# Kernel tuning notes

Hardware: AMD Instinct MI355X
Metric: run time of the kernel (lower is better)

Reference implementation:

```python
import jax, jax.numpy as jnp
import numpy as np

B, T, D_MODEL, HEADS = 2, 2048, 1024, 16
D_HEAD = D_MODEL // HEADS


def setup_inputs() -> dict:
    key = jax.random.key(0)
    ks = jax.random.split(key, 9)
    s = 1.0 / np.sqrt(D_HEAD)
    return {
        "x": jax.random.normal(ks[0], (B, T, D_MODEL), dtype=jnp.float32),
        "Wq": jax.random.normal(ks[1], (D_HEAD, D_HEAD), dtype=jnp.float32) * s,
        "bq": jax.random.normal(ks[2], (D_HEAD,), dtype=jnp.float32) * 0.01,
        "Wk": jax.random.normal(ks[3], (D_HEAD, D_HEAD), dtype=jnp.float32) * s,
        "bk": jax.random.normal(ks[4], (D_HEAD,), dtype=jnp.float32) * 0.01,
        "Wv": jax.random.normal(ks[5], (D_HEAD, D_HEAD), dtype=jnp.float32) * s,
        "bv": jax.random.normal(ks[6], (D_HEAD,), dtype=jnp.float32) * 0.01,
        "Wp": jax.random.normal(ks[7], (D_MODEL, D_MODEL), dtype=jnp.float32) * (1.0 / np.sqrt(D_MODEL)),
        "bp": jax.random.normal(ks[8], (D_MODEL,), dtype=jnp.float32) * 0.01,
    }


def reference(x, Wq, bq, Wk, bk, Wv, bv, Wp, bp):
    b, t, c = x.shape
    xh = x.reshape(b, t, HEADS, D_HEAD)  # [B,T,H,dh]
    # per-head linear projections (weights shared across heads), nn.Linear: y = x @ W.T + b
    q = jnp.einsum('bthd,ed->bhte', xh, Wq) + bq  # [B,H,T,dh]
    k = jnp.einsum('bthd,ed->bhte', xh, Wk) + bk
    v = jnp.einsum('bthd,ed->bhte', xh, Wv) + bv
    # NOTE: original scales by sqrt(C) = sqrt(d_model), not sqrt(d_head)
    scale = 1.0 / jnp.sqrt(jnp.float32(c))
    att = jnp.einsum('bhqd,bhkd->bhqk', q, k) * scale  # [B,H,T,T]
    att = jax.nn.softmax(att, axis=-1)
    out = jnp.einsum('bhqk,bhkd->bhqd', att, v)  # [B,H,T,dh]
    out = out.transpose(0, 2, 1, 3).reshape(b, t, c)  # [B,T,C]
    out = out @ Wp.T + bp
    return out
```

## Files before the change

kernel.cpp:

```cpp
#include <hip/hip_runtime.h>
#include <hip/hip_bf16.h>

#define B_ 2
#define T_ 2048
#define DM_ 1024
#define H_ 16
#define DH_ 64
#define QSCALE 0.045084220027780106f

typedef unsigned short u16;
typedef unsigned int u32;
typedef __attribute__((ext_vector_type(2))) unsigned int u32x2;
typedef __attribute__((ext_vector_type(4))) unsigned int u32x4;
typedef __attribute__((ext_vector_type(4))) float f32x4v;
typedef __attribute__((ext_vector_type(8))) short bf16x8;
typedef __attribute__((ext_vector_type(4))) float f32x4;
typedef __attribute__((ext_vector_type(16))) float f32x16;

__device__ __forceinline__ u16 f2bf(float f) {
    u32 u = __float_as_uint(f);
    return (u16)((u + 0x7FFF + ((u >> 16) & 1)) >> 16);
}
__device__ __forceinline__ float bf2f(u16 h) {
    return __uint_as_float(((u32)h) << 16);
}
__device__ __forceinline__ float exp2_fast(float x) {
    float r;
    asm("v_exp_f32 %0, %1" : "=v"(r) : "v"(x));
    return r;
}
__device__ __forceinline__ u32 cvtpk_bf16(float lo, float hi) {
    u32 r;
    asm("v_cvt_pk_bf16_f32 %0, %1, %2" : "=v"(r) : "v"(lo), "v"(hi));
    return r;
}

__device__ __forceinline__ const bf16x8* frag_at(const u16* base, int row, int c16) {
    return (const bf16x8*)((const char*)base + row * 128 + ((c16 ^ (row & 7)) << 4));
}

__global__ __launch_bounds__(256) void wsplit_all(
    const float* __restrict__ Wq, const float* __restrict__ Wk,
    const float* __restrict__ Wv, const float* __restrict__ Wp,
    u16* __restrict__ W6, u16* __restrict__ Wh, u16* __restrict__ Wl)
{
    const int i = blockIdx.x * 256 + threadIdx.x;
    if (i < DM_ * DM_) {
        const float w = Wp[i];
        const u16 hi = f2bf(w);
        Wh[i] = hi;
        Wl[i] = f2bf(w - bf2f(hi));
    } else {
        const int j = i - DM_ * DM_;
        const int mat = j >> 12, idx = j & 4095;
        const float w = (mat == 0) ? Wq[idx] : (mat == 1) ? Wk[idx] : Wv[idx];
        const u16 hi = f2bf(w);
        W6[(mat * 2) * 4096 + idx] = hi;
        W6[(mat * 2 + 1) * 4096 + idx] = f2bf(w - bf2f(hi));
    }
}

__global__ __launch_bounds__(256) void qkv_mfma(
    const float* __restrict__ x,
    const float* __restrict__ bq, const float* __restrict__ bk,
    const float* __restrict__ bv, const u16* __restrict__ W6,
    u16* __restrict__ Q, u16* __restrict__ K, u16* __restrict__ VT)
{
    __shared__ u16 Ws[6 * 4096];

    const int tid = threadIdx.x;
    const int wid = tid >> 6;
    const int lane = tid & 63;
    const int li = lane & 15, g = lane >> 4;

    const int bh = blockIdx.x >> 4;
    const int t0 = (blockIdx.x & 15) * 128;
    const int b = bh >> 4, h = bh & 15;
    const int tw0 = t0 + wid * 32;

    #pragma unroll
    for (int j = 0; j < 12; ++j) {
        const int gi = j * 256 + tid;
        const int tile = gi >> 9;
        const int t16 = gi & 511;
        const int r = t16 >> 3, c16 = t16 & 7;
        const int c16s = c16 ^ (r & 7);
        __builtin_amdgcn_global_load_lds(
            (const __attribute__((address_space(1))) u32*)((const char*)W6 + tile * 8192 + r * 128 + (c16s << 4)),
            (__attribute__((address_space(3))) u32*)((char*)Ws + gi * 16),
            16, 0, 0);
    }

    const float* xb = x + ((size_t)b * T_) * DM_ + h * 64;
    f32x4v xr[2][2][2];
    #pragma unroll
    for (int mt = 0; mt < 2; ++mt)
        #pragma unroll
        for (int kt = 0; kt < 2; ++kt) {
            const float* p = xb + (size_t)(tw0 + 16 * mt + li) * DM_ + kt * 32 + g * 8;
            xr[mt][kt][0] = *(const f32x4v*)p;
            xr[mt][kt][1] = *(const f32x4v*)(p + 4);
        }

    float bq_r[4], bk_r[4], bv_r[4][4];
    #pragma unroll
    for (int nt = 0; nt < 4; ++nt) { bq_r[nt] = bq[16 * nt + li]; bk_r[nt] = bk[16 * nt + li]; }
    #pragma unroll
    for (int vd = 0; vd < 4; ++vd)
        #pragma unroll
        for (int rg = 0; rg < 4; ++rg) bv_r[vd][rg] = bv[16 * vd + 4 * g + rg];

    __syncthreads();

    bf16x8 xhf[2][2], xlf[2][2];
    #pragma unroll
    for (int mt = 0; mt < 2; ++mt)
        #pragma unroll
        for (int kt = 0; kt < 2; ++kt) {
            u32 hw[4], lw[4];
            #pragma unroll
            for (int q2 = 0; q2 < 2; ++q2) {
                const f32x4v v = xr[mt][kt][q2];
                const u32 p0 = cvtpk_bf16(v[0], v[1]);
                const u32 p1 = cvtpk_bf16(v[2], v[3]);
                const float l0 = v[0] - __uint_as_float(p0 << 16);
                const float l1 = v[1] - __uint_as_float(p0 & 0xFFFF0000u);
                const float l2 = v[2] - __uint_as_float(p1 << 16);
                const float l3 = v[3] - __uint_as_float(p1 & 0xFFFF0000u);
                hw[q2 * 2] = p0; hw[q2 * 2 + 1] = p1;
                lw[q2 * 2] = cvtpk_bf16(l0, l1);
                lw[q2 * 2 + 1] = cvtpk_bf16(l2, l3);
            }
            xhf[mt][kt] = *(const bf16x8*)hw;
            xlf[mt][kt] = *(const bf16x8*)lw;
        }

    const u16* Wqh = Ws;
    const u16* Wql = Ws + 4096;
    const u16* Wkh = Ws + 8192;
    const u16* Wkl = Ws + 12288;
    const u16* Wvh = Ws + 16384;
    const u16* Wvl = Ws + 20480;

    const size_t qk_base = ((size_t)bh * T_) * DH_;

    {
        f32x4 acc[2][4];
        #pragma unroll
        for (int mt = 0; mt < 2; ++mt)
            #pragma unroll
            for (int nt = 0; nt < 4; ++nt) acc[mt][nt] = (f32x4){0.f, 0.f, 0.f, 0.f};
        #pragma unroll
        for (int nt = 0; nt < 4; ++nt)
            #pragma unroll
            for (int kt = 0; kt < 2; ++kt) {
                const bf16x8 wh = *frag_at(Wqh, 16 * nt + li, 4 * kt + g);
                const bf16x8 wl = *frag_at(Wql, 16 * nt + li, 4 * kt + g);
                #pragma unroll
                for (int mt = 0; mt < 2; ++mt) {
                    acc[mt][nt] = __builtin_amdgcn_mfma_f32_16x16x32_bf16(xhf[mt][kt], wh, acc[mt][nt], 0, 0, 0);
                    acc[mt][nt] = __builtin_amdgcn_mfma_f32_16x16x32_bf16(xlf[mt][kt], wh, acc[mt][nt], 0, 0, 0);
                    acc[mt][nt] = __builtin_amdgcn_mfma_f32_16x16x32_bf16(xhf[mt][kt], wl, acc[mt][nt], 0, 0, 0);
                }
            }
        #pragma unroll
        for (int mt = 0; mt < 2; ++mt)
            #pragma unroll
            for (int rg = 0; rg < 4; ++rg) {
                const int t = tw0 + 16 * mt + 4 * g + rg;
                #pragma unroll
                for (int nt = 0; nt < 4; ++nt)
                    Q[qk_base + (size_t)t * DH_ + 16 * nt + li] =
                        f2bf((acc[mt][nt][rg] + bq_r[nt]) * QSCALE);
            }
    }

    {
        f32x4 acc[2][4];
        #pragma unroll
        for (int mt = 0; mt < 2; ++mt)
            #pragma unroll
            for (int nt = 0; nt < 4; ++nt) acc[mt][nt] = (f32x4){0.f, 0.f, 0.f, 0.f};
        #pragma unroll
        for (int nt = 0; nt < 4; ++nt)
            #pragma unroll
            for (int kt = 0; kt < 2; ++kt) {
                const bf16x8 wh = *frag_at(Wkh, 16 * nt + li, 4 * kt + g);
                const bf16x8 wl = *frag_at(Wkl, 16 * nt + li, 4 * kt + g);
                #pragma unroll
                for (int mt = 0; mt < 2; ++mt) {
                    acc[mt][nt] = __builtin_amdgcn_mfma_f32_16x16x32_bf16(xhf[mt][kt], wh, acc[mt][nt], 0, 0, 0);
                    acc[mt][nt] = __builtin_amdgcn_mfma_f32_16x16x32_bf16(xlf[mt][kt], wh, acc[mt][nt], 0, 0, 0);
                    acc[mt][nt] = __builtin_amdgcn_mfma_f32_16x16x32_bf16(xhf[mt][kt], wl, acc[mt][nt], 0, 0, 0);
                }
            }
        #pragma unroll
        for (int mt = 0; mt < 2; ++mt)
            #pragma unroll
            for (int rg = 0; rg < 4; ++rg) {
                const int t = tw0 + 16 * mt + 4 * g + rg;
                #pragma unroll
                for (int nt = 0; nt < 4; ++nt)
                    K[qk_base + (size_t)t * DH_ + 16 * nt + li] =
                        f2bf(acc[mt][nt][rg] + bk_r[nt]);
            }
    }

    {
        f32x4 acc[4][2];
        #pragma unroll
        for (int vd = 0; vd < 4; ++vd)
            #pragma unroll
            for (int tc = 0; tc < 2; ++tc) acc[vd][tc] = (f32x4){0.f, 0.f, 0.f, 0.f};
        #pragma unroll
        for (int vd = 0; vd < 4; ++vd)
            #pragma unroll
            for (int kt = 0; kt < 2; ++kt) {
                const bf16x8 ah = *frag_at(Wvh, 16 * vd + li, 4 * kt + g);
                const bf16x8 al = *frag_at(Wvl, 16 * vd + li, 4 * kt + g);
                #pragma unroll
                for (int tc = 0; tc < 2; ++tc) {
                    acc[vd][tc] = __builtin_amdgcn_mfma_f32_16x16x32_bf16(ah, xhf[tc][kt], acc[vd][tc], 0, 0, 0);
                    acc[vd][tc] = __builtin_amdgcn_mfma_f32_16x16x32_bf16(al, xhf[tc][kt], acc[vd][tc], 0, 0, 0);
                    acc[vd][tc] = __builtin_amdgcn_mfma_f32_16x16x32_bf16(ah, xlf[tc][kt], acc[vd][tc], 0, 0, 0);
                }
            }
        u16* VTb = VT + (size_t)bh * DH_ * T_;
        #pragma unroll
        for (int vd = 0; vd < 4; ++vd)
            #pragma unroll
            for (int rg = 0; rg < 4; ++rg) {
                const int d = 16 * vd + 4 * g + rg;
                #pragma unroll
                for (int tc = 0; tc < 2; ++tc)
                    VTb[(size_t)d * T_ + tw0 + 16 * tc + li] =
                        f2bf(acc[vd][tc][rg] + bv_r[vd][rg]);
            }
    }
}

__global__ __launch_bounds__(256) void attn_mfma(
    const u16* __restrict__ Q, const u16* __restrict__ K,
    const u16* __restrict__ VT, u16* __restrict__ Ah, u16* __restrict__ Al)
{
    __shared__ char smem[32768];

    const int tid = threadIdx.x;
    const int wid = tid >> 6;
    const int lane = tid & 63;
    const int l = lane & 31, h = lane >> 5;
    const int flat = blockIdx.x;
    const int bh = (flat & 7) + ((flat >> 7) << 3);
    const int qx = (flat >> 3) & 15;
    const int q0 = qx * 128 + wid * 32;

    const size_t bhoff = (size_t)bh * T_ * DH_;

    bf16x8 qf[4];
    {
        const u16* Qp = Q + bhoff + (size_t)(q0 + l) * DH_ + 8 * h;
        #pragma unroll
        for (int kt = 0; kt < 4; ++kt)
            qf[kt] = *(const bf16x8*)(Qp + 16 * kt);
    }

    f32x16 o0 = {}, o1 = {};
    float l_part = 0.f;

    const char* ldsR[4];
    #pragma unroll
    for (int kt = 0; kt < 4; ++kt)
        ldsR[kt] = smem + l * 128 + ((((2 * kt + h) ^ (l & 7))) << 4);

    const int sl_r = lane >> 3;
    const int sl_c = (lane & 7) ^ sl_r;
    const char* kgp0 = (const char*)(K + bhoff) + (16 * wid + sl_r) * 128 + (sl_c << 4);
    const char* kgp1 = kgp0 + 8 * 128;
    const char* vgp0 = (const char*)(VT + (size_t)bh * DH_ * T_) + (size_t)(16 * wid + sl_r) * (T_ * 2) + (sl_c << 4);
    const char* vgp1 = vgp0 + (size_t)8 * (T_ * 2);
    const int kdst = 16 * wid * 128 + lane * 16;

#define STAGE(BUF)                                                                       \
    {                                                                                    \
        __builtin_amdgcn_global_load_lds(                                                \
            (const __attribute__((address_space(1))) u32*)kgp0,                          \
            (__attribute__((address_space(3))) u32*)(smem + (BUF) + kdst), 16, 0, 0);    \
        __builtin_amdgcn_global_load_lds(                                                \
            (const __attribute__((address_space(1))) u32*)kgp1,                          \
            (__attribute__((address_space(3))) u32*)(smem + (BUF) + kdst + 1024), 16, 0, 0); \
        __builtin_amdgcn_global_load_lds(                                                \
            (const __attribute__((address_space(1))) u32*)vgp0,                          \
            (__attribute__((address_space(3))) u32*)(smem + 16384 + (BUF) + kdst), 16, 0, 0); \
        __builtin_amdgcn_global_load_lds(                                                \
            (const __attribute__((address_space(1))) u32*)vgp1,                          \
            (__attribute__((address_space(3))) u32*)(smem + 16384 + (BUF) + kdst + 1024), 16, 0, 0); \
        kgp0 += 8192; kgp1 += 8192; vgp0 += 128; vgp1 += 128;                            \
    }

#define ATTN_ITER(BUF, DO_PREF)                                                          \
    {                                                                                    \
        __syncthreads();                                                                 \
        if (DO_PREF) STAGE((BUF) ^ 8192);                                                \
        f32x16 s0 = {}, s1 = {};                                                         \
        __builtin_amdgcn_s_setprio(1);                                                   \
        _Pragma("unroll")                                                                \
        for (int kt = 0; kt < 4; ++kt) {                                                 \
            const bf16x8 kf0 = *(const bf16x8*)(ldsR[kt] + (BUF));                       \
            const bf16x8 kf1 = *(const bf16x8*)(ldsR[kt] + (BUF) + 4096);                \
            s0 = __builtin_amdgcn_mfma_f32_32x32x16_bf16(kf0, qf[kt], s0, 0, 0, 0);      \
            s1 = __builtin_amdgcn_mfma_f32_32x32x16_bf16(kf1, qf[kt], s1, 0, 0, 0);      \
        }                                                                                \
        __builtin_amdgcn_s_setprio(0);                                                   \
        float lacc = 0.f;                                                                \
        _Pragma("unroll")                                                                \
        for (int r = 0; r < 16; ++r) { s0[r] = exp2_fast(s0[r]); lacc += s0[r]; }        \
        _Pragma("unroll")                                                                \
        for (int r = 0; r < 16; ++r) { s1[r] = exp2_fast(s1[r]); lacc += s1[r]; }        \
        l_part += lacc;                                                                  \
        __builtin_amdgcn_s_setprio(1);                                                   \
        _Pragma("unroll")                                                                \
        for (int kt = 0; kt < 4; ++kt) {                                                 \
            const int rb = (kt & 1) * 8;                                                 \
            u32 w0, w1, w2, w3;                                                          \
            if (kt < 2) {                                                                \
                w0 = cvtpk_bf16(s0[rb + 0], s0[rb + 1]);                                 \
                w1 = cvtpk_bf16(s0[rb + 2], s0[rb + 3]);                                 \
                w2 = cvtpk_bf16(s0[rb + 4], s0[rb + 5]);                                 \
                w3 = cvtpk_bf16(s0[rb + 6], s0[rb + 7]);                                 \
            } else {                                                                     \
                w0 = cvtpk_bf16(s1[rb + 0], s1[rb + 1]);                                 \
                w1 = cvtpk_bf16(s1[rb + 2], s1[rb + 3]);                                 \
                w2 = cvtpk_bf16(s1[rb + 4], s1[rb + 5]);                                 \
                w3 = cvtpk_bf16(s1[rb + 6], s1[rb + 7]);                                 \
            }                                                                            \
            asm("v_permlane32_swap_b32 %0, %1" : "+v"(w0), "+v"(w2));                    \
            asm("v_permlane32_swap_b32 %0, %1" : "+v"(w1), "+v"(w3));                    \
            u32x4 pw; pw[0] = w0; pw[1] = w1; pw[2] = w2; pw[3] = w3;                    \
            const bf16x8 pf = __builtin_bit_cast(bf16x8, pw);                            \
            const bf16x8 vf0 = *(const bf16x8*)(ldsR[kt] + 16384 + (BUF));               \
            const bf16x8 vf1 = *(const bf16x8*)(ldsR[kt] + 16384 + (BUF) + 4096);        \
            o0 = __builtin_amdgcn_mfma_f32_32x32x16_bf16(vf0, pf, o0, 0, 0, 0);          \
            o1 = __builtin_amdgcn_mfma_f32_32x32x16_bf16(vf1, pf, o1, 0, 0, 0);          \
        }                                                                                \
        __builtin_amdgcn_s_setprio(0);                                                   \
    }

    STAGE(0);
    for (int it = 0; it < 32; it += 2) {
        ATTN_ITER(0, true);
        ATTN_ITER(8192, (it + 2 < 32));
    }
#undef ATTN_ITER
#undef STAGE

    const float lt = l_part + __shfl_xor(l_part, 32);
    const float inv = 1.0f / lt;

    __syncthreads();

    char* ehi = smem + wid * 8192;
    char* elo = ehi + 4096;
    #pragma unroll
    for (int db = 0; db < 2; ++db) {
        #pragma unroll
        for (int rr = 0; rr < 4; ++rr) {
            float v0, v1, v2, v3;
            if (db == 0) {
                v0 = o0[4 * rr + 0] * inv; v1 = o0[4 * rr + 1] * inv;
                v2 = o0[4 * rr + 2] * inv; v3 = o0[4 * rr + 3] * inv;
            } else {
                v0 = o1[4 * rr + 0] * inv; v1 = o1[4 * rr + 1] * inv;
                v2 = o1[4 * rr + 2] * inv; v3 = o1[4 * rr + 3] * inv;
            }
            u32x2 wh, wl;
            wh.x = cvtpk_bf16(v0, v1);
            wh.y = cvtpk_bf16(v2, v3);
            const float r0 = v0 - __uint_as_float(wh.x << 16);
            const float r1 = v1 - __uint_as_float(wh.x & 0xFFFF0000u);
            const float r2 = v2 - __uint_as_float(wh.y << 16);
            const float r3 = v3 - __uint_as_float(wh.y & 0xFFFF0000u);
            wl.x = cvtpk_bf16(r0, r1);
            wl.y = cvtpk_bf16(r2, r3);
            const int byteoff = l * 128 + (((4 * db + rr) ^ (l & 7)) << 4) + 8 * h;
            *(u32x2*)(ehi + byteoff) = wh;
            *(u32x2*)(elo + byteoff) = wl;
        }
    }

    const int b = bh >> 4, head = bh & 15;
    const int sub = lane & 7;
    const int row8 = lane >> 3;
    #pragma unroll
    for (int rr = 0; rr < 4; ++rr) {
        const int row = 8 * rr + row8;
        const int byteoff = row * 128 + ((sub ^ row8) << 4);
        const size_t gidx = ((size_t)b * T_ + q0 + row) * DM_ + head * 64 + sub * 8;
        *(u32x4*)(Ah + gidx) = *(const u32x4*)(ehi + byteoff);
        *(u32x4*)(Al + gidx) = *(const u32x4*)(elo + byteoff);
    }
}

__global__ __launch_bounds__(512) void proj_mfma(
    const u16* __restrict__ Ah, const u16* __restrict__ Al,
    const u16* __restrict__ Wh, const u16* __restrict__ Wl,
    const float* __restrict__ bp, float* __restrict__ out)
{
    __shared__ char smem[131072];

    const int tid = threadIdx.x;
    const int wid = tid >> 6;
    const int lane = tid & 63;
    const int li = lane & 15, g = lane >> 4;
    const int row0 = blockIdx.y * 128, col0 = blockIdx.x * 128;

    const int mat = wid >> 1, half = wid & 1;
    const char* gsrc;
    if (mat == 0)      gsrc = (const char*)(Ah + (size_t)row0 * DM_);
    else if (mat == 1) gsrc = (const char*)(Al + (size_t)row0 * DM_);
    else if (mat == 2) gsrc = (const char*)(Wh + (size_t)col0 * DM_);
    else               gsrc = (const char*)(Wl + (size_t)col0 * DM_);
    const int r_local = half * 64 + (lane >> 3);
    const int c16s = (lane & 7) ^ (lane >> 3);
    const char* gp0 = gsrc + (size_t)r_local * (DM_ * 2) + (c16s << 4);
    const int ldst0 = mat * 16384 + half * 8192;

#define PSTAGE(BUF, STEP)                                                                \
    {                                                                                    \
        _Pragma("unroll")                                                                \
        for (int j = 0; j < 8; ++j) {                                                    \
            __builtin_amdgcn_global_load_lds(                                            \
                (const __attribute__((address_space(1))) u32*)(gp0 + (size_t)(STEP) * 128 + (size_t)j * (8 * DM_ * 2)), \
                (__attribute__((address_space(3))) u32*)(smem + (BUF) + ldst0 + j * 1024),\
                16, 0, 0);                                                               \
        }                                                                                \
    }

    const int wr = wid >> 1, wc = wid & 1;

    f32x4 acc[2][4];
    #pragma unroll
    for (int m = 0; m < 2; ++m)
        #pragma unroll
        for (int n = 0; n < 4; ++n) acc[m][n] = (f32x4){0.f, 0.f, 0.f, 0.f};

    PSTAGE(0, 0);
    for (int step = 0; step < 16; ++step) {
        const int buf = (step & 1) * 65536;
        __syncthreads();
        if (step < 15) PSTAGE(buf ^ 65536, step + 1);

        const u16* pAh = (const u16*)(smem + buf);
        const u16* pAl = (const u16*)(smem + buf + 16384);
        const u16* pWh = (const u16*)(smem + buf + 32768);
        const u16* pWl = (const u16*)(smem + buf + 49152);

        __builtin_amdgcn_s_setprio(1);
        #pragma unroll
        for (int kt = 0; kt < 2; ++kt) {
            bf16x8 ah[2], al[2], wh[4], wl[4];
            #pragma unroll
            for (int m = 0; m < 2; ++m) {
                ah[m] = *frag_at(pAh, wr * 32 + m * 16 + li, kt * 4 + g);
                al[m] = *frag_at(pAl, wr * 32 + m * 16 + li, kt * 4 + g);
            }
            #pragma unroll
            for (int n = 0; n < 4; ++n) {
                wh[n] = *frag_at(pWh, wc * 64 + n * 16 + li, kt * 4 + g);
                wl[n] = *frag_at(pWl, wc * 64 + n * 16 + li, kt * 4 + g);
            }
            #pragma unroll
            for (int m = 0; m < 2; ++m)
                #pragma unroll
                for (int n = 0; n < 4; ++n) {
                    acc[m][n] = __builtin_amdgcn_mfma_f32_16x16x32_bf16(ah[m], wh[n], acc[m][n], 0, 0, 0);
                    acc[m][n] = __builtin_amdgcn_mfma_f32_16x16x32_bf16(al[m], wh[n], acc[m][n], 0, 0, 0);
                    acc[m][n] = __builtin_amdgcn_mfma_f32_16x16x32_bf16(ah[m], wl[n], acc[m][n], 0, 0, 0);
                }
        }
        __builtin_amdgcn_s_setprio(0);
    }
#undef PSTAGE

    const int orow = row0 + wr * 32;
    const int ocol = col0 + wc * 64;
    float bias[4];
    #pragma unroll
    for (int n = 0; n < 4; ++n) bias[n] = bp[ocol + n * 16 + li];
    #pragma unroll
    for (int m = 0; m < 2; ++m)
        #pragma unroll
        for (int n = 0; n < 4; ++n)
            #pragma unroll
            for (int q = 0; q < 4; ++q)
                out[(size_t)(orow + m * 16 + g * 4 + q) * DM_ + ocol + n * 16 + li] =
                    acc[m][n][q] + bias[n];
}

extern "C" void kernel_launch(void* const* d_in, const int* in_sizes, int n_in,
                              void* d_out, int out_size, void* d_ws, size_t ws_size,
                              hipStream_t stream) {
    const float* x  = (const float*)d_in[0];
    const float* Wq = (const float*)d_in[1];
    const float* bq = (const float*)d_in[2];
    const float* Wk = (const float*)d_in[3];
    const float* bk = (const float*)d_in[4];
    const float* Wv = (const float*)d_in[5];
    const float* bv = (const float*)d_in[6];
    const float* Wp = (const float*)d_in[7];
    const float* bp = (const float*)d_in[8];
    float* out = (float*)d_out;

    const size_t n_qkv = (size_t)B_ * H_ * T_ * DH_;
    const size_t n_w   = (size_t)DM_ * DM_;
    u16* Qb  = (u16*)d_ws;
    u16* Kb  = Qb + n_qkv;
    u16* VTb = Kb + n_qkv;
    u16* Ahb = VTb + n_qkv;
    u16* Alb = Ahb + n_qkv;
    u16* Whb = Alb + n_qkv;
    u16* Wlb = Whb + n_w;
    u16* W6b = Wlb + n_w;

    wsplit_all<<<(n_w + 12288) / 256, 256, 0, stream>>>(Wq, Wk, Wv, Wp, W6b, Whb, Wlb);
    qkv_mfma<<<32 * 16, 256, 0, stream>>>(x, bq, bk, bv, W6b, Qb, Kb, VTb);
    attn_mfma<<<512, 256, 0, stream>>>(Qb, Kb, VTb, Ahb, Alb);
    proj_mfma<<<dim3(DM_ / 128, (B_ * T_) / 128), 512, 0, stream>>>(Ahb, Alb, Whb, Wlb, bp, out);
}
```

Baseline: 91.27 us.

## Split attention KV range across two blocks and add a combine kernel

Each attention block now covers half of the key/value sequence, so the grid doubles to 1024 blocks. Partial unnormalized outputs and row sums go to fp32 workspace, and a new combine kernel sums the halves, normalizes, and writes the hi/lo bf16 split, reusing the Q/K buffers as outputs. The main loop is also restructured to software-pipeline QK for the next tile with softmax/PV of the current one, using separate K and V staging. This raises occupancy and overlap at the cost of extra global traffic for the fp32 partials and one more kernel launch.

```diff
diff --git a/kernel.cpp b/kernel.cpp
--- a/kernel.cpp
+++ b/kernel.cpp
@@ -241,7 +241,7 @@
 
 __global__ __launch_bounds__(256) void attn_mfma(
     const u16* __restrict__ Q, const u16* __restrict__ K,
-    const u16* __restrict__ VT, u16* __restrict__ Ah, u16* __restrict__ Al)
+    const u16* __restrict__ VT, float* __restrict__ OP, float* __restrict__ LP)
 {
     __shared__ char smem[32768];
 
@@ -250,8 +250,9 @@
     const int lane = tid & 63;
     const int l = lane & 31, h = lane >> 5;
     const int flat = blockIdx.x;
-    const int bh = (flat & 7) + ((flat >> 7) << 3);
-    const int qx = (flat >> 3) & 15;
+    const int gid = flat & 63;
+    const int bh = gid >> 1, kvh = gid & 1;
+    const int qx = flat >> 6;
     const int q0 = qx * 128 + wid * 32;
 
     const size_t bhoff = (size_t)bh * T_ * DH_;
@@ -265,6 +266,7 @@
     }
 
     f32x16 o0 = {}, o1 = {};
+    f32x16 s0A = {}, s1A = {}, s0B = {}, s1B = {};
     float l_part = 0.f;
 
     const char* ldsR[4];
@@ -274,48 +276,55 @@
 
     const int sl_r = lane >> 3;
     const int sl_c = (lane & 7) ^ sl_r;
-    const char* kgp0 = (const char*)(K + bhoff) + (16 * wid + sl_r) * 128 + (sl_c << 4);
+    const char* kgp0 = (const char*)(K + bhoff) + kvh * 131072 + (16 * wid + sl_r) * 128 + (sl_c << 4);
     const char* kgp1 = kgp0 + 8 * 128;
-    const char* vgp0 = (const char*)(VT + (size_t)bh * DH_ * T_) + (size_t)(16 * wid + sl_r) * (T_ * 2) + (sl_c << 4);
+    const char* vgp0 = (const char*)(VT + (size_t)bh * DH_ * T_) + kvh * 2048 + (size_t)(16 * wid + sl_r) * (T_ * 2) + (sl_c << 4);
     const char* vgp1 = vgp0 + (size_t)8 * (T_ * 2);
     const int kdst = 16 * wid * 128 + lane * 16;
 
-#define STAGE(BUF)                                                                       \
+#define STAGE_K(DST)                                                                     \
     {                                                                                    \
         __builtin_amdgcn_global_load_lds(                                                \
             (const __attribute__((address_space(1))) u32*)kgp0,                          \
-            (__attribute__((address_space(3))) u32*)(smem + (BUF) + kdst), 16, 0, 0);    \
+            (__attribute__((address_space(3))) u32*)(smem + (DST) + kdst), 16, 0, 0);    \
         __builtin_amdgcn_global_load_lds(                                                \
             (const __attribute__((address_space(1))) u32*)kgp1,                          \
-            (__attribute__((address_space(3))) u32*)(smem + (BUF) + kdst + 1024), 16, 0, 0); \
+            (__attribute__((address_space(3))) u32*)(smem + (DST) + kdst + 1024), 16, 0, 0); \
+        kgp0 += 8192; kgp1 += 8192;                                                      \
+    }
+#define STAGE_V(DST)                                                                     \
+    {                                                                                    \
         __builtin_amdgcn_global_load_lds(                                                \
             (const __attribute__((address_space(1))) u32*)vgp0,                          \
-            (__attribute__((address_space(3))) u32*)(smem + 16384 + (BUF) + kdst), 16, 0, 0); \
+            (__attribute__((address_space(3))) u32*)(smem + (DST) + kdst), 16, 0, 0);    \
         __builtin_amdgcn_global_load_lds(                                                \
             (const __attribute__((address_space(1))) u32*)vgp1,                          \
-            (__attribute__((address_space(3))) u32*)(smem + 16384 + (BUF) + kdst + 1024), 16, 0, 0); \
-        kgp0 += 8192; kgp1 += 8192; vgp0 += 128; vgp1 += 128;                            \
-    }
-
-#define ATTN_ITER(BUF, DO_PREF)                                                          \
+            (__attribute__((address_space(3))) u32*)(smem + (DST) + kdst + 1024), 16, 0, 0); \
+        vgp0 += 128; vgp1 += 128;                                                        \
+    }
+
+#define QK_BLOCK(KB, S0, S1)                                                             \
     {                                                                                    \
-        __syncthreads();                                                                 \
-        if (DO_PREF) STAGE((BUF) ^ 8192);                                                \
-        f32x16 s0 = {}, s1 = {};                                                         \
+        S0 = (f32x16){}; S1 = (f32x16){};                                                \
         __builtin_amdgcn_s_setprio(1);                                                   \
         _Pragma("unroll")                                                                \
         for (int kt = 0; kt < 4; ++kt) {                                                 \
-            const bf16x8 kf0 = *(const bf16x8*)(ldsR[kt] + (BUF));                       \
-            const bf16x8 kf1 = *(const bf16x8*)(ldsR[kt] + (BUF) + 4096);                \
-            s0 = __builtin_amdgcn_mfma_f32_32x32x16_bf16(kf0, qf[kt], s0, 0, 0, 0);      \
-            s1 = __builtin_amdgcn_mfma_f32_32x32x16_bf16(kf1, qf[kt], s1, 0, 0, 0);      \
+            const bf16x8 kf0 = *(const bf16x8*)(ldsR[kt] + (KB));                        \
+            const bf16x8 kf1 = *(const bf16x8*)(ldsR[kt] + (KB) + 4096);                 \
+            S0 = __builtin_amdgcn_mfma_f32_32x32x16_bf16(kf0, qf[kt], S0, 0, 0, 0);      \
+            S1 = __builtin_amdgcn_mfma_f32_32x32x16_bf16(kf1, qf[kt], S1, 0, 0, 0);      \
         }                                                                                \
         __builtin_amdgcn_s_setprio(0);                                                   \
+        __builtin_amdgcn_sched_barrier(0);                                               \
+    }
+
+#define SOFTMAX_PV(S0, S1, VB)                                                           \
+    {                                                                                    \
         float lacc = 0.f;                                                                \
         _Pragma("unroll")                                                                \
-        for (int r = 0; r < 16; ++r) { s0[r] = exp2_fast(s0[r]); lacc += s0[r]; }        \
+        for (int r = 0; r < 16; ++r) { S0[r] = exp2_fast(S0[r]); lacc += S0[r]; }        \
         _Pragma("unroll")                                                                \
-        for (int r = 0; r < 16; ++r) { s1[r] = exp2_fast(s1[r]); lacc += s1[r]; }        \
+        for (int r = 0; r < 16; ++r) { S1[r] = exp2_fast(S1[r]); lacc += S1[r]; }        \
         l_part += lacc;                                                                  \
         __builtin_amdgcn_s_setprio(1);                                                   \
         _Pragma("unroll")                                                                \
@@ -323,81 +332,131 @@
             const int rb = (kt & 1) * 8;                                                 \
             u32 w0, w1, w2, w3;                                                          \
             if (kt < 2) {                                                                \
-                w0 = cvtpk_bf16(s0[rb + 0], s0[rb + 1]);                                 \
-                w1 = cvtpk_bf16(s0[rb + 2], s0[rb + 3]);                                 \
-                w2 = cvtpk_bf16(s0[rb + 4], s0[rb + 5]);                                 \
-                w3 = cvtpk_bf16(s0[rb + 6], s0[rb + 7]);                                 \
+                w0 = cvtpk_bf16(S0[rb + 0], S0[rb + 1]);                                 \
+                w1 = cvtpk_bf16(S0[rb + 2], S0[rb + 3]);                                 \
+                w2 = cvtpk_bf16(S0[rb + 4], S0[rb + 5]);                                 \
+                w3 = cvtpk_bf16(S0[rb + 6], S0[rb + 7]);                                 \
             } else {                                                                     \
-                w0 = cvtpk_bf16(s1[rb + 0], s1[rb + 1]);                                 \
-                w1 = cvtpk_bf16(s1[rb + 2], s1[rb + 3]);                                 \
-                w2 = cvtpk_bf16(s1[rb + 4], s1[rb + 5]);                                 \
-                w3 = cvtpk_bf16(s1[rb + 6], s1[rb + 7]);                                 \
+                w0 = cvtpk_bf16(S1[rb + 0], S1[rb + 1]);                                 \
+                w1 = cvtpk_bf16(S1[rb + 2], S1[rb + 3]);                                 \
+                w2 = cvtpk_bf16(S1[rb + 4], S1[rb + 5]);                                 \
+                w3 = cvtpk_bf16(S1[rb + 6], S1[rb + 7]);                                 \
             }                                                                            \
             asm("v_permlane32_swap_b32 %0, %1" : "+v"(w0), "+v"(w2));                    \
             asm("v_permlane32_swap_b32 %0, %1" : "+v"(w1), "+v"(w3));                    \
             u32x4 pw; pw[0] = w0; pw[1] = w1; pw[2] = w2; pw[3] = w3;                    \
             const bf16x8 pf = __builtin_bit_cast(bf16x8, pw);                            \
-            const bf16x8 vf0 = *(const bf16x8*)(ldsR[kt] + 16384 + (BUF));               \
-            const bf16x8 vf1 = *(const bf16x8*)(ldsR[kt] + 16384 + (BUF) + 4096);        \
+            const bf16x8 vf0 = *(const bf16x8*)(ldsR[kt] + (VB));                        \
+            const bf16x8 vf1 = *(const bf16x8*)(ldsR[kt] + (VB) + 4096);                 \
             o0 = __builtin_amdgcn_mfma_f32_32x32x16_bf16(vf0, pf, o0, 0, 0, 0);          \
             o1 = __builtin_amdgcn_mfma_f32_32x32x16_bf16(vf1, pf, o1, 0, 0, 0);          \
         }                                                                                \
         __builtin_amdgcn_s_setprio(0);                                                   \
     }
 
-    STAGE(0);
-    for (int it = 0; it < 32; it += 2) {
-        ATTN_ITER(0, true);
-        ATTN_ITER(8192, (it + 2 < 32));
-    }
-#undef ATTN_ITER
-#undef STAGE
+    STAGE_K(0);
+    STAGE_V(16384);
+    __syncthreads();
+    QK_BLOCK(0, s0A, s1A);
+    STAGE_K(8192);
+
+    for (int it = 0; it < 16; it += 2) {
+        __syncthreads();
+        if (it + 2 < 16) STAGE_K(0);
+        STAGE_V(24576);
+        QK_BLOCK(8192, s0B, s1B);
+        SOFTMAX_PV(s0A, s1A, 16384);
+
+        __syncthreads();
+        if (it + 3 < 16) STAGE_K(8192);
+        if (it + 2 < 16) {
+            STAGE_V(16384);
+            QK_BLOCK(0, s0A, s1A);
+        }
+        SOFTMAX_PV(s0B, s1B, 24576);
+    }
+#undef STAGE_K
+#undef STAGE_V
+#undef QK_BLOCK
+#undef SOFTMAX_PV
 
     const float lt = l_part + __shfl_xor(l_part, 32);
-    const float inv = 1.0f / lt;
 
     __syncthreads();
 
-    char* ehi = smem + wid * 8192;
-    char* elo = ehi + 4096;
+    float* ew = (float*)(smem + wid * 8192);
     #pragma unroll
     for (int db = 0; db < 2; ++db) {
         #pragma unroll
         for (int rr = 0; rr < 4; ++rr) {
-            float v0, v1, v2, v3;
+            f32x4v v;
             if (db == 0) {
-                v0 = o0[4 * rr + 0] * inv; v1 = o0[4 * rr + 1] * inv;
-                v2 = o0[4 * rr + 2] * inv; v3 = o0[4 * rr + 3] * inv;
+                v[0] = o0[4 * rr + 0]; v[1] = o0[4 * rr + 1];
+                v[2] = o0[4 * rr + 2]; v[3] = o0[4 * rr + 3];
             } else {
-                v0 = o1[4 * rr + 0] * inv; v1 = o1[4 * rr + 1] * inv;
-                v2 = o1[4 * rr + 2] * inv; v3 = o1[4 * rr + 3] * inv;
-            }
-            u32x2 wh, wl;
-            wh.x = cvtpk_bf16(v0, v1);
-            wh.y = cvtpk_bf16(v2, v3);
-            const float r0 = v0 - __uint_as_float(wh.x << 16);
-            const float r1 = v1 - __uint_as_float(wh.x & 0xFFFF0000u);
-            const float r2 = v2 - __uint_as_float(wh.y << 16);
-            const float r3 = v3 - __uint_as_float(wh.y & 0xFFFF0000u);
-            wl.x = cvtpk_bf16(r0, r1);
-            wl.y = cvtpk_bf16(r2, r3);
-            const int byteoff = l * 128 + (((4 * db + rr) ^ (l & 7)) << 4) + 8 * h;
-            *(u32x2*)(ehi + byteoff) = wh;
-            *(u32x2*)(elo + byteoff) = wl;
+                v[0] = o1[4 * rr + 0]; v[1] = o1[4 * rr + 1];
+                v[2] = o1[4 * rr + 2]; v[3] = o1[4 * rr + 3];
+            }
+            const int gr = (2 * rr + h + 8 * db) ^ (l & 15);
+            *(f32x4v*)((char*)ew + l * 256 + (gr << 4)) = v;
         }
     }
 
-    const int b = bh >> 4, head = bh & 15;
-    const int sub = lane & 7;
-    const int row8 = lane >> 3;
-    #pragma unroll
-    for (int rr = 0; rr < 4; ++rr) {
-        const int row = 8 * rr + row8;
-        const int byteoff = row * 128 + ((sub ^ row8) << 4);
-        const size_t gidx = ((size_t)b * T_ + q0 + row) * DM_ + head * 64 + sub * 8;
-        *(u32x4*)(Ah + gidx) = *(const u32x4*)(ehi + byteoff);
-        *(u32x4*)(Al + gidx) = *(const u32x4*)(elo + byteoff);
-    }
+    const size_t rowbase = (size_t)bh * T_ + q0;
+    float* opb = OP + (size_t)kvh * (65536ull * 64);
+    const int ql = lane >> 1, hf = lane & 1;
+    float* oprow = opb + (rowbase + ql) * 64 + hf * 32;
+    #pragma unroll
+    for (int j = 0; j < 8; ++j) {
+        const int gr = (hf * 8 + j) ^ (ql & 15);
+        const f32x4v v = *(const f32x4v*)((char*)ew + ql * 256 + (gr << 4));
+        *(f32x4v*)(oprow + 4 * j) = v;
+    }
+    if (h == 0) LP[kvh * 65536 + rowbase + l] = lt;
+}
+
+__global__ __launch_bounds__(256) void combine_kernel(
+    const float* __restrict__ OP, const float* __restrict__ LP,
+    u16* __restrict__ Ah, u16* __restrict__ Al)
+{
+    const int tid = threadIdx.x;
+    const int row = blockIdx.x * 64 + (tid >> 2);
+    const int dq = (tid & 3) * 16;
+    const float inv = 1.0f / (LP[row] + LP[65536 + row]);
+    const float* p0 = OP + (size_t)row * 64 + dq;
+    const float* p1 = p0 + 65536ull * 64;
+    const int bh = row >> 11, q = row & 2047;
+    const int b = bh >> 4, hh = bh & 15;
+    const size_t gidx = ((size_t)(b * T_ + q)) * DM_ + hh * 64 + dq;
+
+    u32 hw[8], lw[8];
+    #pragma unroll
+    for (int j = 0; j < 4; ++j) {
+        const f32x4v a = *(const f32x4v*)(p0 + 4 * j);
+        const f32x4v c = *(const f32x4v*)(p1 + 4 * j);
+        const float v0 = (a[0] + c[0]) * inv;
+        const float v1 = (a[1] + c[1]) * inv;
+        const float v2 = (a[2] + c[2]) * inv;
+        const float v3 = (a[3] + c[3]) * inv;
+        const u32 h0 = cvtpk_bf16(v0, v1);
+        const u32 h1 = cvtpk_bf16(v2, v3);
+        const float r0 = v0 - __uint_as_float(h0 << 16);
+        const float r1 = v1 - __uint_as_float(h0 & 0xFFFF0000u);
+        const float r2 = v2 - __uint_as_float(h1 << 16);
+        const float r3 = v3 - __uint_as_float(h1 & 0xFFFF0000u);
+        hw[2 * j] = h0; hw[2 * j + 1] = h1;
+        lw[2 * j] = cvtpk_bf16(r0, r1);
+        lw[2 * j + 1] = cvtpk_bf16(r2, r3);
+    }
+    u32x4 hv0, hv1, lv0, lv1;
+    hv0[0] = hw[0]; hv0[1] = hw[1]; hv0[2] = hw[2]; hv0[3] = hw[3];
+    hv1[0] = hw[4]; hv1[1] = hw[5]; hv1[2] = hw[6]; hv1[3] = hw[7];
+    lv0[0] = lw[0]; lv0[1] = lw[1]; lv0[2] = lw[2]; lv0[3] = lw[3];
+    lv1[0] = lw[4]; lv1[1] = lw[5]; lv1[2] = lw[6]; lv1[3] = lw[7];
+    *(u32x4*)(Ah + gidx) = hv0;
+    *(u32x4*)(Ah + gidx + 8) = hv1;
+    *(u32x4*)(Al + gidx) = lv0;
+    *(u32x4*)(Al + gidx + 8) = lv1;
 }
 
 __global__ __launch_bounds__(512) void proj_mfma(
@@ -515,14 +574,15 @@
     u16* Qb  = (u16*)d_ws;
     u16* Kb  = Qb + n_qkv;
     u16* VTb = Kb + n_qkv;
-    u16* Ahb = VTb + n_qkv;
-    u16* Alb = Ahb + n_qkv;
-    u16* Whb = Alb + n_qkv;
+    u16* Whb = VTb + n_qkv;
     u16* Wlb = Whb + n_w;
     u16* W6b = Wlb + n_w;
+    float* OPb = (float*)(W6b + 24576);
+    float* LPb = OPb + 2 * n_qkv;
 
     wsplit_all<<<(n_w + 12288) / 256, 256, 0, stream>>>(Wq, Wk, Wv, Wp, W6b, Whb, Wlb);
     qkv_mfma<<<32 * 16, 256, 0, stream>>>(x, bq, bk, bv, W6b, Qb, Kb, VTb);
-    attn_mfma<<<512, 256, 0, stream>>>(Qb, Kb, VTb, Ahb, Alb);
-    proj_mfma<<<dim3(DM_ / 128, (B_ * T_) / 128), 512, 0, stream>>>(Ahb, Alb, Whb, Wlb, bp, out);
-}
+    attn_mfma<<<1024, 256, 0, stream>>>(Qb, Kb, VTb, OPb, LPb);
+    combine_kernel<<<1024, 256, 0, stream>>>(OPb, LPb, Qb, Kb);
+    proj_mfma<<<dim3(DM_ / 128, (B_ * T_) / 128), 512, 0, stream>>>(Qb, Kb, Whb, Wlb, bp, out);
+}
```

New measurement: 106.5 us. 16.7% more time.

## Double the attention KV tile to 128 keys per iteration

Applied to the files above, without the earlier changes.

The attention main loop now processes 128 keys per iteration instead of 64. LDS doubles to 64KB to hold double-buffered K and V tiles, and the iteration count halves. This halves the number of block barriers and prefetch stages per key and exposes four independent QK MFMA chains before the softmax/PV phase. In exchange it adds register pressure from four live score accumulators, and the larger LDS footprint may cut the number of resident blocks per CU.

```diff
diff --git a/kernel.cpp b/kernel.cpp
--- a/kernel.cpp
+++ b/kernel.cpp
@@ -243,7 +243,7 @@
     const u16* __restrict__ Q, const u16* __restrict__ K,
     const u16* __restrict__ VT, u16* __restrict__ Ah, u16* __restrict__ Al)
 {
-    __shared__ char smem[32768];
+    __shared__ char smem[65536];
 
     const int tid = threadIdx.x;
     const int wid = tid >> 6;
@@ -265,92 +265,99 @@
     }
 
     f32x16 o0 = {}, o1 = {};
+    f32x16 sA, sB, sC, sD;
     float l_part = 0.f;
 
     const char* ldsR[4];
     #pragma unroll
-    for (int kt = 0; kt < 4; ++kt)
-        ldsR[kt] = smem + l * 128 + ((((2 * kt + h) ^ (l & 7))) << 4);
+    for (int j = 0; j < 4; ++j)
+        ldsR[j] = smem + l * 128 + ((((2 * j + h) ^ (l & 7))) << 4);
 
     const int sl_r = lane >> 3;
     const int sl_c = (lane & 7) ^ sl_r;
-    const char* kgp0 = (const char*)(K + bhoff) + (16 * wid + sl_r) * 128 + (sl_c << 4);
-    const char* kgp1 = kgp0 + 8 * 128;
-    const char* vgp0 = (const char*)(VT + (size_t)bh * DH_ * T_) + (size_t)(16 * wid + sl_r) * (T_ * 2) + (sl_c << 4);
-    const char* vgp1 = vgp0 + (size_t)8 * (T_ * 2);
-    const int kdst = 16 * wid * 128 + lane * 16;
-
-#define STAGE(BUF)                                                                       \
+    const char* kgp = (const char*)(K + bhoff) + (32 * wid + sl_r) * 128 + (sl_c << 4);
+    const char* vgp = (const char*)(VT + (size_t)bh * DH_ * T_) + (size_t)(16 * wid + sl_r) * (T_ * 2) + (sl_c << 4);
+    const int kdst = 32 * wid * 128 + lane * 16;
+    const int vdst = 16 * wid * 128 + lane * 16;
+
+#define STAGE(KB_, VB_)                                                                  \
     {                                                                                    \
+        _Pragma("unroll")                                                                \
+        for (int j = 0; j < 4; ++j)                                                      \
+            __builtin_amdgcn_global_load_lds(                                            \
+                (const __attribute__((address_space(1))) u32*)(kgp + j * 1024),          \
+                (__attribute__((address_space(3))) u32*)(smem + (KB_) + kdst + j * 1024),\
+                16, 0, 0);                                                               \
         __builtin_amdgcn_global_load_lds(                                                \
-            (const __attribute__((address_space(1))) u32*)kgp0,                          \
-            (__attribute__((address_space(3))) u32*)(smem + (BUF) + kdst), 16, 0, 0);    \
+            (const __attribute__((address_space(1))) u32*)vgp,                           \
+            (__attribute__((address_space(3))) u32*)(smem + (VB_) + vdst), 16, 0, 0);    \
         __builtin_amdgcn_global_load_lds(                                                \
-            (const __attribute__((address_space(1))) u32*)kgp1,                          \
-            (__attribute__((address_space(3))) u32*)(smem + (BUF) + kdst + 1024), 16, 0, 0); \
+            (const __attribute__((address_space(1))) u32*)(vgp + 8 * T_ * 2),            \
+            (__attribute__((address_space(3))) u32*)(smem + (VB_) + vdst + 1024), 16, 0, 0); \
         __builtin_amdgcn_global_load_lds(                                                \
-            (const __attribute__((address_space(1))) u32*)vgp0,                          \
-            (__attribute__((address_space(3))) u32*)(smem + 16384 + (BUF) + kdst), 16, 0, 0); \
+            (const __attribute__((address_space(1))) u32*)(vgp + 128),                   \
+            (__attribute__((address_space(3))) u32*)(smem + (VB_) + 8192 + vdst), 16, 0, 0); \
         __builtin_amdgcn_global_load_lds(                                                \
-            (const __attribute__((address_space(1))) u32*)vgp1,                          \
-            (__attribute__((address_space(3))) u32*)(smem + 16384 + (BUF) + kdst + 1024), 16, 0, 0); \
-        kgp0 += 8192; kgp1 += 8192; vgp0 += 128; vgp1 += 128;                            \
-    }
-
-#define ATTN_ITER(BUF, DO_PREF)                                                          \
+            (const __attribute__((address_space(1))) u32*)(vgp + 8 * T_ * 2 + 128),      \
+            (__attribute__((address_space(3))) u32*)(smem + (VB_) + 8192 + vdst + 1024), 16, 0, 0); \
+        kgp += 16384; vgp += 256;                                                        \
+    }
+
+#define QK(KB_, S, c)                                                                    \
     {                                                                                    \
-        __syncthreads();                                                                 \
-        if (DO_PREF) STAGE((BUF) ^ 8192);                                                \
-        f32x16 s0 = {}, s1 = {};                                                         \
-        __builtin_amdgcn_s_setprio(1);                                                   \
+        S = (f32x16){};                                                                  \
         _Pragma("unroll")                                                                \
         for (int kt = 0; kt < 4; ++kt) {                                                 \
-            const bf16x8 kf0 = *(const bf16x8*)(ldsR[kt] + (BUF));                       \
-            const bf16x8 kf1 = *(const bf16x8*)(ldsR[kt] + (BUF) + 4096);                \
-            s0 = __builtin_amdgcn_mfma_f32_32x32x16_bf16(kf0, qf[kt], s0, 0, 0, 0);      \
-            s1 = __builtin_amdgcn_mfma_f32_32x32x16_bf16(kf1, qf[kt], s1, 0, 0, 0);      \
+            const bf16x8 kf = *(const bf16x8*)(ldsR[kt] + (KB_) + (c) * 4096);           \
+            S = __builtin_amdgcn_mfma_f32_32x32x16_bf16(kf, qf[kt], S, 0, 0, 0);         \
         }                                                                                \
-        __builtin_amdgcn_s_setprio(0);                                                   \
+    }
+
+#define SMPV(S, c, VB_)                                                                  \
+    {                                                                                    \
         float lacc = 0.f;                                                                \
         _Pragma("unroll")                                                                \
-        for (int r = 0; r < 16; ++r) { s0[r] = exp2_fast(s0[r]); lacc += s0[r]; }        \
-        _Pragma("unroll")                                                                \
-        for (int r = 0; r < 16; ++r) { s1[r] = exp2_fast(s1[r]); lacc += s1[r]; }        \
+        for (int r = 0; r < 16; ++r) { S[r] = exp2_fast(S[r]); lacc += S[r]; }           \
         l_part += lacc;                                                                  \
         __builtin_amdgcn_s_setprio(1);                                                   \
         _Pragma("unroll")                                                                \
-        for (int kt = 0; kt < 4; ++kt) {                                                 \
-            const int rb = (kt & 1) * 8;                                                 \
-            u32 w0, w1, w2, w3;                                                          \
-            if (kt < 2) {                                                                \
-                w0 = cvtpk_bf16(s0[rb + 0], s0[rb + 1]);                                 \
-                w1 = cvtpk_bf16(s0[rb + 2], s0[rb + 3]);                                 \
-                w2 = cvtpk_bf16(s0[rb + 4], s0[rb + 5]);                                 \
-                w3 = cvtpk_bf16(s0[rb + 6], s0[rb + 7]);                                 \
-            } else {                                                                     \
-                w0 = cvtpk_bf16(s1[rb + 0], s1[rb + 1]);                                 \
-                w1 = cvtpk_bf16(s1[rb + 2], s1[rb + 3]);                                 \
-                w2 = cvtpk_bf16(s1[rb + 4], s1[rb + 5]);                                 \
-                w3 = cvtpk_bf16(s1[rb + 6], s1[rb + 7]);                                 \
-            }                                                                            \
+        for (int ktl = 0; ktl < 2; ++ktl) {                                              \
+            const int rb = ktl * 8;                                                      \
+            u32 w0 = cvtpk_bf16(S[rb + 0], S[rb + 1]);                                   \
+            u32 w1 = cvtpk_bf16(S[rb + 2], S[rb + 3]);                                   \
+            u32 w2 = cvtpk_bf16(S[rb + 4], S[rb + 5]);                                   \
+            u32 w3 = cvtpk_bf16(S[rb + 6], S[rb + 7]);                                   \
             asm("v_permlane32_swap_b32 %0, %1" : "+v"(w0), "+v"(w2));                    \
             asm("v_permlane32_swap_b32 %0, %1" : "+v"(w1), "+v"(w3));                    \
             u32x4 pw; pw[0] = w0; pw[1] = w1; pw[2] = w2; pw[3] = w3;                    \
             const bf16x8 pf = __builtin_bit_cast(bf16x8, pw);                            \
-            const bf16x8 vf0 = *(const bf16x8*)(ldsR[kt] + 16384 + (BUF));               \
-            const bf16x8 vf1 = *(const bf16x8*)(ldsR[kt] + 16384 + (BUF) + 4096);        \
+            const char* vb = ldsR[2 * ((c) & 1) + ktl] + (VB_) + ((c) >> 1) * 8192;      \
+            const bf16x8 vf0 = *(const bf16x8*)vb;                                       \
+            const bf16x8 vf1 = *(const bf16x8*)(vb + 4096);                              \
             o0 = __builtin_amdgcn_mfma_f32_32x32x16_bf16(vf0, pf, o0, 0, 0, 0);          \
             o1 = __builtin_amdgcn_mfma_f32_32x32x16_bf16(vf1, pf, o1, 0, 0, 0);          \
         }                                                                                \
         __builtin_amdgcn_s_setprio(0);                                                   \
     }
 
-    STAGE(0);
-    for (int it = 0; it < 32; it += 2) {
-        ATTN_ITER(0, true);
-        ATTN_ITER(8192, (it + 2 < 32));
+#define ATTN_ITER(KB_, VB_, PKB_, PVB_, DO_PREF)                                         \
+    {                                                                                    \
+        __syncthreads();                                                                 \
+        if (DO_PREF) STAGE(PKB_, PVB_);                                                  \
+        __builtin_amdgcn_s_setprio(1);                                                   \
+        QK(KB_, sA, 0); QK(KB_, sB, 1); QK(KB_, sC, 2); QK(KB_, sD, 3);                  \
+        __builtin_amdgcn_s_setprio(0);                                                   \
+        SMPV(sA, 0, VB_); SMPV(sB, 1, VB_); SMPV(sC, 2, VB_); SMPV(sD, 3, VB_);          \
+    }
+
+    STAGE(0, 32768);
+    for (int it = 0; it < 16; it += 2) {
+        ATTN_ITER(0, 32768, 16384, 49152, true);
+        ATTN_ITER(16384, 49152, 0, 32768, (it + 2 < 16));
     }
 #undef ATTN_ITER
+#undef SMPV
+#undef QK
 #undef STAGE
 
     const float lt = l_part + __shfl_xor(l_part, 32);
```

Result: no change. 90.12 us (-1.3%).
